# Optimization experiments

Hardware: AMD Instinct MI355X
Metric: run time of the kernel (lower is better)

## Reference

```python
import jax, jax.numpy as jnp
import numpy as np

K1, K2 = 2, 4  # kernels of the two channel groups
BN_EPS = 1e-5


def _neocell_group(x, wa, wb, k):
    # Block-diagonal (a @ x) @ b with a k x k block repeated along the diagonal
    # per channel (NeoCellRepeat): equivalent to blockwise transforms on H and W.
    B, c, H, W = x.shape
    xb = x.reshape(B, c, H // k, k, W // k, k)
    y = jnp.einsum('cpi,bcnimj,cjq->bcnpmq', wa, xb, wb)
    return y.reshape(B, c, H, W)


def setup_inputs() -> dict:
    key = jax.random.key(0)
    ks = jax.random.split(key, 12)
    B, C, H, W = 32, 256, 56, 56
    c1, c2 = 128, 128
    Ci = 4 * C  # inner_mult = 4
    x = jax.random.normal(ks[0], (B, C, H, W), dtype=jnp.float32)
    wa1 = jax.random.normal(ks[1], (c1, K1, K1), dtype=jnp.float32) / np.float32(np.sqrt(K1))
    wb1 = jax.random.normal(ks[2], (c1, K1, K1), dtype=jnp.float32) / np.float32(np.sqrt(K1))
    wa2 = jax.random.normal(ks[3], (c2, K2, K2), dtype=jnp.float32) / np.float32(np.sqrt(K2))
    wb2 = jax.random.normal(ks[4], (c2, K2, K2), dtype=jnp.float32) / np.float32(np.sqrt(K2))
    bn_weight = 1.0 + 0.1 * jax.random.normal(ks[5], (C,), dtype=jnp.float32)
    bn_bias = 0.1 * jax.random.normal(ks[6], (C,), dtype=jnp.float32)
    bn_mean = 0.1 * jax.random.normal(ks[7], (C,), dtype=jnp.float32)
    bn_var = jax.random.uniform(ks[8], (C,), dtype=jnp.float32, minval=0.5, maxval=1.5)
    fc1_w = jax.random.normal(ks[9], (Ci, C), dtype=jnp.float32) / np.float32(np.sqrt(C))
    fc2_w = jax.random.normal(ks[10], (C, Ci), dtype=jnp.float32) / np.float32(np.sqrt(Ci))
    return {"x": x, "wa1": wa1, "wb1": wb1, "wa2": wa2, "wb2": wb2,
            "bn_weight": bn_weight, "bn_bias": bn_bias, "bn_mean": bn_mean,
            "bn_var": bn_var, "fc1_w": fc1_w, "fc2_w": fc2_w}


def reference(x, wa1, wb1, wa2, wb2, bn_weight, bn_bias, bn_mean, bn_var, fc1_w, fc2_w):
    c1 = wa1.shape[0]
    # NeoCell: per-group block-diagonal (a @ x) @ b
    y = jnp.concatenate([
        _neocell_group(x[:, :c1], wa1, wb1, K1),
        _neocell_group(x[:, c1:], wa2, wb2, K2),
    ], axis=1)
    # BatchNorm2d (eval mode, running stats)
    inv = jax.lax.rsqrt(bn_var + BN_EPS)
    scale = (bn_weight * inv)[None, :, None, None]
    shift = (bn_bias - bn_mean * bn_weight * inv)[None, :, None, None]
    y = y * scale + shift
    # chw -> hwc, MLP with exact GELU, hwc -> chw
    y = jnp.transpose(y, (0, 2, 3, 1))
    h = jax.nn.gelu(y @ fc1_w.T, approximate=False)
    y = h @ fc2_w.T
    y = jnp.transpose(y, (0, 3, 1, 2))
    # residual (drop_path = 0)
    return y + x
```

## Files before the change

### kernel.cpp

```cpp
#include <hip/hip_runtime.h>
#include <stdint.h>

typedef __bf16 bf16x8 __attribute__((ext_vector_type(8)));
typedef float f32x4 __attribute__((ext_vector_type(4)));

__device__ __forceinline__ float bf2f(uint16_t u) {
  union { uint32_t i; float f; } v; v.i = ((uint32_t)u) << 16; return v.f;
}
__device__ __forceinline__ uint16_t f2bf(float f) {
  union { float f; uint32_t i; } v; v.f = f;
  uint32_t u = v.i;
  uint32_t r = (u + 0x7FFFu + ((u >> 16) & 1u)) >> 16;
  return (uint16_t)r;
}
__device__ __forceinline__ float fast_gelu(float v) {
  float t2 = v * v;
  float pz = 1.0f + 0.044715f * t2;
  float w = -1.5957691216f * v * pz;
  float e = __expf(w);
  return v * __builtin_amdgcn_rcpf(1.0f + e);
}

__global__ __launch_bounds__(256) void cvt_weights_kernel(
    const float* __restrict__ fc1, const float* __restrict__ fc2,
    uint16_t* __restrict__ fc1b, uint16_t* __restrict__ fc2b)
{
  int i = (blockIdx.x * 256 + threadIdx.x) * 4;
  if (i < 262144) {
    float4 a = *(const float4*)(fc1 + i);
    ushort4 o;
    o.x = f2bf(a.x); o.y = f2bf(a.y); o.z = f2bf(a.z); o.w = f2bf(a.w);
    *(ushort4*)(fc1b + i) = o;
  } else {
    int j = i - 262144;
    float4 a = *(const float4*)(fc2 + j);
    ushort4 o;
    o.x = f2bf(a.x); o.y = f2bf(a.y); o.z = f2bf(a.z); o.w = f2bf(a.w);
    *(ushort4*)(fc2b + j) = o;
  }
}

__global__ __launch_bounds__(128) void neocell_bn_kernel(
    const float* __restrict__ x,
    const float* __restrict__ wa1, const float* __restrict__ wb1,
    const float* __restrict__ wa2, const float* __restrict__ wb2,
    const float* __restrict__ bnw, const float* __restrict__ bnb,
    const float* __restrict__ bnm, const float* __restrict__ bnv,
    uint16_t* __restrict__ y1)
{
  __shared__ uint16_t lx[128 * 226];
  const int t = threadIdx.x;
  const int strip = blockIdx.x;
  const int b = blockIdx.y;
  const int half = blockIdx.z;
  const int h0 = strip * 4;

  for (int i = 0; i < 56; ++i) {
    int l = t + i * 128;
    int c = l / 56;
    int r = l - c * 56;
    const float* g = x + (size_t)(b * 256 + half * 128 + c) * 3136
                       + h0 * 56 + r * 4;
    float4 v = *(const float4*)g;
    ushort4 o;
    o.x = f2bf(v.x); o.y = f2bf(v.y); o.z = f2bf(v.z); o.w = f2bf(v.w);
    *(ushort4*)(lx + c * 226 + r * 4) = o;
  }
  __syncthreads();

  const int a = t & 63;
  const int p = t >> 6;
  const int c0 = half * 128 + 2 * a;

  float sc[2], sh[2];
#pragma unroll
  for (int ch = 0; ch < 2; ++ch) {
    int cg = c0 + ch;
    sc[ch] = bnw[cg] * rsqrtf(bnv[cg] + 1e-5f);
    sh[ch] = bnb[cg] - bnm[cg] * sc[ch];
  }
  const size_t pgbase = (size_t)b * 3136 + (size_t)h0 * 56;

  if (half == 0) {
    float A[2][2][2], Bm[2][2][2];
#pragma unroll
    for (int ch = 0; ch < 2; ++ch)
#pragma unroll
      for (int i = 0; i < 2; ++i)
#pragma unroll
        for (int j = 0; j < 2; ++j) {
          A[ch][i][j]  = wa1[(2 * a + ch) * 4 + i * 2 + j];
          Bm[ch][i][j] = wb1[(2 * a + ch) * 4 + i * 2 + j];
        }
    for (int m = 0; m < 28; ++m) {
      float O[2][2][2];
#pragma unroll
      for (int ch = 0; ch < 2; ++ch) {
        const uint16_t* lc = lx + (2 * a + ch) * 226 + (2 * p) * 56 + m * 2;
        uint32_t w0 = *(const uint32_t*)lc;
        uint32_t w1 = *(const uint32_t*)(lc + 56);
        float X[2][2];
        X[0][0] = bf2f((uint16_t)w0); X[0][1] = bf2f((uint16_t)(w0 >> 16));
        X[1][0] = bf2f((uint16_t)w1); X[1][1] = bf2f((uint16_t)(w1 >> 16));
        float T[2][2];
#pragma unroll
        for (int pp = 0; pp < 2; ++pp)
#pragma unroll
          for (int j = 0; j < 2; ++j)
            T[pp][j] = A[ch][pp][0] * X[0][j] + A[ch][pp][1] * X[1][j];
#pragma unroll
        for (int pp = 0; pp < 2; ++pp)
#pragma unroll
          for (int q = 0; q < 2; ++q)
            O[ch][pp][q] = (T[pp][0] * Bm[ch][0][q] + T[pp][1] * Bm[ch][1][q])
                           * sc[ch] + sh[ch];
      }
#pragma unroll
      for (int pp = 0; pp < 2; ++pp)
#pragma unroll
        for (int q = 0; q < 2; ++q) {
          uint32_t pk = (uint32_t)f2bf(O[0][pp][q])
                      | ((uint32_t)f2bf(O[1][pp][q]) << 16);
          size_t pg = pgbase + (size_t)(2 * p + pp) * 56 + (m * 2 + q);
          *(uint32_t*)(y1 + pg * 256 + c0) = pk;
        }
    }
  } else {
    float A[2][4][4], Bm[2][4][4];
#pragma unroll
    for (int ch = 0; ch < 2; ++ch)
#pragma unroll
      for (int i = 0; i < 4; ++i)
#pragma unroll
        for (int j = 0; j < 4; ++j) {
          A[ch][i][j]  = wa2[(2 * a + ch) * 16 + i * 4 + j];
          Bm[ch][i][j] = wb2[(2 * a + ch) * 16 + i * 4 + j];
        }
    for (int mm = 0; mm < 7; ++mm) {
      int m = 2 * mm + p;
      float O[2][4][4];
#pragma unroll
      for (int ch = 0; ch < 2; ++ch) {
        float X[4][4];
#pragma unroll
        for (int i = 0; i < 4; ++i) {
          const uint16_t* lc = lx + (2 * a + ch) * 226 + i * 56 + m * 4;
          uint32_t w0 = *(const uint32_t*)lc;
          uint32_t w1 = *(const uint32_t*)(lc + 2);
          X[i][0] = bf2f((uint16_t)w0); X[i][1] = bf2f((uint16_t)(w0 >> 16));
          X[i][2] = bf2f((uint16_t)w1); X[i][3] = bf2f((uint16_t)(w1 >> 16));
        }
        float T[4][4];
#pragma unroll
        for (int pp = 0; pp < 4; ++pp)
#pragma unroll
          for (int j = 0; j < 4; ++j)
            T[pp][j] = A[ch][pp][0] * X[0][j] + A[ch][pp][1] * X[1][j]
                     + A[ch][pp][2] * X[2][j] + A[ch][pp][3] * X[3][j];
#pragma unroll
        for (int pp = 0; pp < 4; ++pp)
#pragma unroll
          for (int q = 0; q < 4; ++q)
            O[ch][pp][q] = (T[pp][0] * Bm[ch][0][q] + T[pp][1] * Bm[ch][1][q]
                          + T[pp][2] * Bm[ch][2][q] + T[pp][3] * Bm[ch][3][q])
                           * sc[ch] + sh[ch];
      }
#pragma unroll
      for (int pp = 0; pp < 4; ++pp)
#pragma unroll
        for (int q = 0; q < 4; ++q) {
          uint32_t pk = (uint32_t)f2bf(O[0][pp][q])
                      | ((uint32_t)f2bf(O[1][pp][q]) << 16);
          size_t pg = pgbase + (size_t)pp * 56 + (m * 4 + q);
          *(uint32_t*)(y1 + pg * 256 + c0) = pk;
        }
    }
  }
}

template <int KD, int EPI>
__global__ __launch_bounds__(256) void gemm_bt_kernel(
    const uint16_t* __restrict__ A,
    const uint16_t* __restrict__ Bw,
    uint16_t* __restrict__ Cb16,
    float* __restrict__ Cf32,
    const float* __restrict__ Xres,
    int chunk_pix0)
{
  __shared__ uint16_t lds[16640];
  uint16_t* ldsA = lds;
  uint16_t* ldsB = lds + 4096;

  const int tid = threadIdx.x;
  const int lane = tid & 63;
  const int wid = tid >> 6;
  const int wm = wid & 1;
  const int wn = wid >> 1;
  const int fm = lane & 15;
  const int fq = lane >> 4;

  const size_t arow0 = (size_t)blockIdx.y * 128;
  const size_t brow0 = (size_t)blockIdx.x * 128;

  f32x4 acc[4][4];
#pragma unroll
  for (int i = 0; i < 4; ++i)
#pragma unroll
    for (int j = 0; j < 4; ++j) { f32x4 z = {0.f, 0.f, 0.f, 0.f}; acc[i][j] = z; }

  const int q0 = tid, q1 = tid + 256;
  const int r0 = q0 >> 2, kk0 = q0 & 3;
  const int r1 = q1 >> 2, kk1 = q1 & 3;
  const uint16_t* a0 = A + (arow0 + r0) * KD + kk0 * 8;
  const uint16_t* a1 = A + (arow0 + r1) * KD + kk1 * 8;
  const uint16_t* b0 = Bw + (brow0 + r0) * KD + kk0 * 8;
  const uint16_t* b1 = Bw + (brow0 + r1) * KD + kk1 * 8;

  for (int k0 = 0; k0 < KD; k0 += 32) {
    __syncthreads();
    __builtin_amdgcn_global_load_lds(
        (const __attribute__((address_space(1))) void*)(a0 + k0),
        (__attribute__((address_space(3))) void*)(ldsA + q0 * 8), 16, 0, 0);
    __builtin_amdgcn_global_load_lds(
        (const __attribute__((address_space(1))) void*)(a1 + k0),
        (__attribute__((address_space(3))) void*)(ldsA + q1 * 8), 16, 0, 0);
    __builtin_amdgcn_global_load_lds(
        (const __attribute__((address_space(1))) void*)(b0 + k0),
        (__attribute__((address_space(3))) void*)(ldsB + q0 * 8), 16, 0, 0);
    __builtin_amdgcn_global_load_lds(
        (const __attribute__((address_space(1))) void*)(b1 + k0),
        (__attribute__((address_space(3))) void*)(ldsB + q1 * 8), 16, 0, 0);
    __syncthreads();

    bf16x8 af[4], bfr[4];
#pragma unroll
    for (int mt = 0; mt < 4; ++mt)
      af[mt] = *(const bf16x8*)(const void*)
               (ldsA + (wm * 64 + mt * 16 + fm) * 32 + fq * 8);
#pragma unroll
    for (int nt = 0; nt < 4; ++nt)
      bfr[nt] = *(const bf16x8*)(const void*)
                (ldsB + (wn * 64 + nt * 16 + fm) * 32 + fq * 8);
#pragma unroll
    for (int mt = 0; mt < 4; ++mt)
#pragma unroll
      for (int nt = 0; nt < 4; ++nt)
        acc[mt][nt] = __builtin_amdgcn_mfma_f32_16x16x32_bf16(
            af[mt], bfr[nt], acc[mt][nt], 0, 0, 0);
  }

  if (EPI == 0) {
#pragma unroll
    for (int mt = 0; mt < 4; ++mt) {
      const size_t rb = arow0 + wm * 64 + mt * 16 + fq * 4;
#pragma unroll
      for (int nt = 0; nt < 4; ++nt) {
        const size_t n = brow0 + wn * 64 + nt * 16 + fm;
#pragma unroll
        for (int r = 0; r < 4; ++r)
          Cb16[(rb + r) * 1024 + n] = f2bf(fast_gelu(acc[mt][nt][r]));
      }
    }
  } else {
    __syncthreads();
#pragma unroll
    for (int mt = 0; mt < 4; ++mt) {
      int mbase = wm * 64 + mt * 16 + fq * 4;
#pragma unroll
      for (int nt = 0; nt < 4; ++nt) {
        int n = wn * 64 + nt * 16 + fm;
#pragma unroll
        for (int r = 0; r < 4; ++r)
          lds[n * 130 + mbase + r] = f2bf(acc[mt][nt][r]);
      }
    }
    __syncthreads();
    const int pl0 = tid & 31;
    const int cw = tid >> 5;
#pragma unroll
    for (int it = 0; it < 16; ++it) {
      int ch = cw + it * 8;
      int cgl = (int)brow0 + ch;
#pragma unroll
      for (int e = 0; e < 4; ++e) {
        int pl = pl0 + e * 32;
        uint32_t pg = (uint32_t)chunk_pix0 + blockIdx.y * 128u + (uint32_t)pl;
        uint32_t bimg = pg / 3136u;
        uint32_t rem = pg - bimg * 3136u;
        size_t addr = ((size_t)bimg * 256 + cgl) * 3136 + rem;
        Cf32[addr] = bf2f(lds[ch * 130 + pl]) + Xres[addr];
      }
    }
  }
}

extern "C" void kernel_launch(void* const* d_in, const int* in_sizes, int n_in,
                              void* d_out, int out_size, void* d_ws,
                              size_t ws_size, hipStream_t stream)
{
  const float* x   = (const float*)d_in[0];
  const float* wa1 = (const float*)d_in[1];
  const float* wb1 = (const float*)d_in[2];
  const float* wa2 = (const float*)d_in[3];
  const float* wb2 = (const float*)d_in[4];
  const float* bnw = (const float*)d_in[5];
  const float* bnb = (const float*)d_in[6];
  const float* bnm = (const float*)d_in[7];
  const float* bnv = (const float*)d_in[8];
  const float* fc1 = (const float*)d_in[9];
  const float* fc2 = (const float*)d_in[10];
  float* out = (float*)d_out;

  uint16_t* fc1b = (uint16_t*)d_ws;
  uint16_t* fc2b = fc1b + 262144;
  uint16_t* y1 = fc2b + 262144;
  const size_t y1_elems = (size_t)100352 * 256;
  uint16_t* h = y1 + y1_elems;

  const long tiles_total = 784;
  const size_t fixed_bytes = (size_t)262144 * 4 + y1_elems * 2;
  long tiles_chunk = 1;
  if (ws_size > fixed_bytes + 262144) {
    tiles_chunk = (long)((ws_size - fixed_bytes) / (128ul * 1024ul * 2ul));
    if (tiles_chunk > tiles_total) tiles_chunk = tiles_total;
    if (tiles_chunk < 1) tiles_chunk = 1;
  }

  cvt_weights_kernel<<<512, 256, 0, stream>>>(fc1, fc2, fc1b, fc2b);
  neocell_bn_kernel<<<dim3(14, 32, 2), 128, 0, stream>>>(
      x, wa1, wb1, wa2, wb2, bnw, bnb, bnm, bnv, y1);

  for (long t0 = 0; t0 < tiles_total; t0 += tiles_chunk) {
    long T = tiles_total - t0;
    if (T > tiles_chunk) T = tiles_chunk;
    gemm_bt_kernel<256, 0><<<dim3(8, (uint32_t)T), 256, 0, stream>>>(
        y1 + (size_t)t0 * 128 * 256, fc1b, h, nullptr, nullptr, 0);
    gemm_bt_kernel<1024, 1><<<dim3(2, (uint32_t)T), 256, 0, stream>>>(
        h, fc2b, nullptr, out, x, (int)(t0 * 128));
  }
}
```

Measured before the change: 443.1 us.

## Fuse fc1+GELU and fc2 GEMMs into one kernel keeping hidden tile in LDS

```diff
diff --git a/kernel.cpp b/kernel.cpp
--- a/kernel.cpp
+++ b/kernel.cpp
@@ -20,6 +20,10 @@
   float e = __expf(w);
   return v * __builtin_amdgcn_rcpf(1.0f + e);
 }
+
+#define GLL(gp, lp) __builtin_amdgcn_global_load_lds( \
+    (const __attribute__((address_space(1))) void*)(gp), \
+    (__attribute__((address_space(3))) void*)(lp), 16, 0, 0)
 
 __global__ __launch_bounds__(256) void cvt_weights_kernel(
     const float* __restrict__ fc1, const float* __restrict__ fc2,
@@ -178,18 +182,17 @@
   }
 }
 
-template <int KD, int EPI>
-__global__ __launch_bounds__(256) void gemm_bt_kernel(
-    const uint16_t* __restrict__ A,
-    const uint16_t* __restrict__ Bw,
-    uint16_t* __restrict__ Cb16,
-    float* __restrict__ Cf32,
-    const float* __restrict__ Xres,
-    int chunk_pix0)
+__global__ __launch_bounds__(256, 2) void fused_mlp_kernel(
+    const uint16_t* __restrict__ y1,
+    const uint16_t* __restrict__ fc1b,
+    const uint16_t* __restrict__ fc2b,
+    const float* __restrict__ x,
+    float* __restrict__ out)
 {
-  __shared__ uint16_t lds[16640];
+  __shared__ uint16_t lds[24576];
   uint16_t* ldsA = lds;
   uint16_t* ldsB = lds + 4096;
+  uint16_t* hbuf = lds + 8192;
 
   const int tid = threadIdx.x;
   const int lane = tid & 63;
@@ -199,97 +202,124 @@
   const int fm = lane & 15;
   const int fq = lane >> 4;
 
-  const size_t arow0 = (size_t)blockIdx.y * 128;
-  const size_t brow0 = (size_t)blockIdx.x * 128;
-
-  f32x4 acc[4][4];
+  const int coh = blockIdx.x;
+  const size_t pix0 = (size_t)blockIdx.y * 128;
+
+  f32x4 oacc[4][4];
 #pragma unroll
   for (int i = 0; i < 4; ++i)
 #pragma unroll
-    for (int j = 0; j < 4; ++j) { f32x4 z = {0.f, 0.f, 0.f, 0.f}; acc[i][j] = z; }
+    for (int j = 0; j < 4; ++j) { f32x4 z = {0.f, 0.f, 0.f, 0.f}; oacc[i][j] = z; }
 
   const int q0 = tid, q1 = tid + 256;
   const int r0 = q0 >> 2, kk0 = q0 & 3;
   const int r1 = q1 >> 2, kk1 = q1 & 3;
-  const uint16_t* a0 = A + (arow0 + r0) * KD + kk0 * 8;
-  const uint16_t* a1 = A + (arow0 + r1) * KD + kk1 * 8;
-  const uint16_t* b0 = Bw + (brow0 + r0) * KD + kk0 * 8;
-  const uint16_t* b1 = Bw + (brow0 + r1) * KD + kk1 * 8;
-
-  for (int k0 = 0; k0 < KD; k0 += 32) {
-    __syncthreads();
-    __builtin_amdgcn_global_load_lds(
-        (const __attribute__((address_space(1))) void*)(a0 + k0),
-        (__attribute__((address_space(3))) void*)(ldsA + q0 * 8), 16, 0, 0);
-    __builtin_amdgcn_global_load_lds(
-        (const __attribute__((address_space(1))) void*)(a1 + k0),
-        (__attribute__((address_space(3))) void*)(ldsA + q1 * 8), 16, 0, 0);
-    __builtin_amdgcn_global_load_lds(
-        (const __attribute__((address_space(1))) void*)(b0 + k0),
-        (__attribute__((address_space(3))) void*)(ldsB + q0 * 8), 16, 0, 0);
-    __builtin_amdgcn_global_load_lds(
-        (const __attribute__((address_space(1))) void*)(b1 + k0),
-        (__attribute__((address_space(3))) void*)(ldsB + q1 * 8), 16, 0, 0);
-    __syncthreads();
-
-    bf16x8 af[4], bfr[4];
-#pragma unroll
-    for (int mt = 0; mt < 4; ++mt)
-      af[mt] = *(const bf16x8*)(const void*)
-               (ldsA + (wm * 64 + mt * 16 + fm) * 32 + fq * 8);
-#pragma unroll
-    for (int nt = 0; nt < 4; ++nt)
-      bfr[nt] = *(const bf16x8*)(const void*)
-                (ldsB + (wn * 64 + nt * 16 + fm) * 32 + fq * 8);
-#pragma unroll
-    for (int mt = 0; mt < 4; ++mt)
+
+  const uint16_t* a0 = y1 + (pix0 + r0) * 256 + kk0 * 8;
+  const uint16_t* a1 = y1 + (pix0 + r1) * 256 + kk1 * 8;
+  const uint16_t* f20 = fc2b + ((size_t)coh * 128 + r0) * 1024 + kk0 * 8;
+  const uint16_t* f21 = fc2b + ((size_t)coh * 128 + r1) * 1024 + kk1 * 8;
+
+  for (int c = 0; c < 8; ++c) {
+    const int hc0 = c * 128;
+    const uint16_t* b0 = fc1b + (size_t)(hc0 + r0) * 256 + kk0 * 8;
+    const uint16_t* b1 = fc1b + (size_t)(hc0 + r1) * 256 + kk1 * 8;
+
+    f32x4 hacc[4][4];
+#pragma unroll
+    for (int i = 0; i < 4; ++i)
+#pragma unroll
+      for (int j = 0; j < 4; ++j) { f32x4 z = {0.f, 0.f, 0.f, 0.f}; hacc[i][j] = z; }
+
+    for (int k0 = 0; k0 < 256; k0 += 32) {
+      __syncthreads();
+      GLL(a0 + k0, ldsA + q0 * 8);
+      GLL(a1 + k0, ldsA + q1 * 8);
+      GLL(b0 + k0, ldsB + q0 * 8);
+      GLL(b1 + k0, ldsB + q1 * 8);
+      __syncthreads();
+
+      bf16x8 af[4], bfr[4];
+#pragma unroll
+      for (int mt = 0; mt < 4; ++mt)
+        af[mt] = *(const bf16x8*)(const void*)
+                 (ldsA + (wm * 64 + mt * 16 + fm) * 32 + fq * 8);
 #pragma unroll
       for (int nt = 0; nt < 4; ++nt)
-        acc[mt][nt] = __builtin_amdgcn_mfma_f32_16x16x32_bf16(
-            af[mt], bfr[nt], acc[mt][nt], 0, 0, 0);
-  }
-
-  if (EPI == 0) {
+        bfr[nt] = *(const bf16x8*)(const void*)
+                  (ldsB + (wn * 64 + nt * 16 + fm) * 32 + fq * 8);
+#pragma unroll
+      for (int mt = 0; mt < 4; ++mt)
+#pragma unroll
+        for (int nt = 0; nt < 4; ++nt)
+          hacc[mt][nt] = __builtin_amdgcn_mfma_f32_16x16x32_bf16(
+              af[mt], bfr[nt], hacc[mt][nt], 0, 0, 0);
+    }
+
 #pragma unroll
     for (int mt = 0; mt < 4; ++mt) {
-      const size_t rb = arow0 + wm * 64 + mt * 16 + fq * 4;
+      int pixl = wm * 64 + mt * 16 + fq * 4;
 #pragma unroll
       for (int nt = 0; nt < 4; ++nt) {
-        const size_t n = brow0 + wn * 64 + nt * 16 + fm;
+        int hcl = wn * 64 + nt * 16 + fm;
+        uint16_t* hp = hbuf + ((hcl >> 5) << 12) + (hcl & 31);
 #pragma unroll
         for (int r = 0; r < 4; ++r)
-          Cb16[(rb + r) * 1024 + n] = f2bf(fast_gelu(acc[mt][nt][r]));
+          hp[(pixl + r) * 32] = f2bf(fast_gelu(hacc[mt][nt][r]));
       }
     }
-  } else {
-    __syncthreads();
-#pragma unroll
-    for (int mt = 0; mt < 4; ++mt) {
-      int mbase = wm * 64 + mt * 16 + fq * 4;
-#pragma unroll
-      for (int nt = 0; nt < 4; ++nt) {
-        int n = wn * 64 + nt * 16 + fm;
-#pragma unroll
-        for (int r = 0; r < 4; ++r)
-          lds[n * 130 + mbase + r] = f2bf(acc[mt][nt][r]);
-      }
-    }
-    __syncthreads();
-    const int pl0 = tid & 31;
-    const int cw = tid >> 5;
-#pragma unroll
-    for (int it = 0; it < 16; ++it) {
-      int ch = cw + it * 8;
-      int cgl = (int)brow0 + ch;
-#pragma unroll
-      for (int e = 0; e < 4; ++e) {
-        int pl = pl0 + e * 32;
-        uint32_t pg = (uint32_t)chunk_pix0 + blockIdx.y * 128u + (uint32_t)pl;
-        uint32_t bimg = pg / 3136u;
-        uint32_t rem = pg - bimg * 3136u;
-        size_t addr = ((size_t)bimg * 256 + cgl) * 3136 + rem;
-        Cf32[addr] = bf2f(lds[ch * 130 + pl]) + Xres[addr];
-      }
+
+    for (int kp = 0; kp < 4; ++kp) {
+      __syncthreads();
+      GLL(f20 + hc0 + kp * 32, ldsB + q0 * 8);
+      GLL(f21 + hc0 + kp * 32, ldsB + q1 * 8);
+      __syncthreads();
+
+      bf16x8 haf[4], cfr[4];
+#pragma unroll
+      for (int mt = 0; mt < 4; ++mt)
+        haf[mt] = *(const bf16x8*)(const void*)
+                  (hbuf + (kp << 12) + (wm * 64 + mt * 16 + fm) * 32 + fq * 8);
+#pragma unroll
+      for (int nt = 0; nt < 4; ++nt)
+        cfr[nt] = *(const bf16x8*)(const void*)
+                  (ldsB + (wn * 64 + nt * 16 + fm) * 32 + fq * 8);
+#pragma unroll
+      for (int mt = 0; mt < 4; ++mt)
+#pragma unroll
+        for (int nt = 0; nt < 4; ++nt)
+          oacc[mt][nt] = __builtin_amdgcn_mfma_f32_16x16x32_bf16(
+              haf[mt], cfr[nt], oacc[mt][nt], 0, 0, 0);
+    }
+  }
+
+  __syncthreads();
+#pragma unroll
+  for (int mt = 0; mt < 4; ++mt) {
+    int mbase = wm * 64 + mt * 16 + fq * 4;
+#pragma unroll
+    for (int nt = 0; nt < 4; ++nt) {
+      int n = wn * 64 + nt * 16 + fm;
+#pragma unroll
+      for (int r = 0; r < 4; ++r)
+        lds[n * 130 + mbase + r] = f2bf(oacc[mt][nt][r]);
+    }
+  }
+  __syncthreads();
+  const int pl0 = tid & 31;
+  const int cw = tid >> 5;
+#pragma unroll
+  for (int it = 0; it < 16; ++it) {
+    int ch = cw + it * 8;
+    int cgl = coh * 128 + ch;
+#pragma unroll
+    for (int e = 0; e < 4; ++e) {
+      int pl = pl0 + e * 32;
+      uint32_t pg = (uint32_t)pix0 + (uint32_t)pl;
+      uint32_t bimg = pg / 3136u;
+      uint32_t rem = pg - bimg * 3136u;
+      size_t addr = ((size_t)bimg * 256 + cgl) * 3136 + rem;
+      out[addr] = bf2f(lds[ch * 130 + pl]) + x[addr];
     }
   }
 }
@@ -314,28 +344,9 @@
   uint16_t* fc1b = (uint16_t*)d_ws;
   uint16_t* fc2b = fc1b + 262144;
   uint16_t* y1 = fc2b + 262144;
-  const size_t y1_elems = (size_t)100352 * 256;
-  uint16_t* h = y1 + y1_elems;
-
-  const long tiles_total = 784;
-  const size_t fixed_bytes = (size_t)262144 * 4 + y1_elems * 2;
-  long tiles_chunk = 1;
-  if (ws_size > fixed_bytes + 262144) {
-    tiles_chunk = (long)((ws_size - fixed_bytes) / (128ul * 1024ul * 2ul));
-    if (tiles_chunk > tiles_total) tiles_chunk = tiles_total;
-    if (tiles_chunk < 1) tiles_chunk = 1;
-  }
 
   cvt_weights_kernel<<<512, 256, 0, stream>>>(fc1, fc2, fc1b, fc2b);
   neocell_bn_kernel<<<dim3(14, 32, 2), 128, 0, stream>>>(
       x, wa1, wb1, wa2, wb2, bnw, bnb, bnm, bnv, y1);
-
-  for (long t0 = 0; t0 < tiles_total; t0 += tiles_chunk) {
-    long T = tiles_total - t0;
-    if (T > tiles_chunk) T = tiles_chunk;
-    gemm_bt_kernel<256, 0><<<dim3(8, (uint32_t)T), 256, 0, stream>>>(
-        y1 + (size_t)t0 * 128 * 256, fc1b, h, nullptr, nullptr, 0);
-    gemm_bt_kernel<1024, 1><<<dim3(2, (uint32_t)T), 256, 0, stream>>>(
-        h, fc2b, nullptr, out, x, (int)(t0 * 128));
-  }
-}
+  fused_mlp_kernel<<<dim3(2, 784), 256, 0, stream>>>(y1, fc1b, fc2b, x, out);
+}
```

New measurement: 506.0 us. +14.2%, slower.
